# Optimization experiments

Hardware: AMD Instinct MI355X
Metric: run time of the kernel (lower is better)

## Reference

```python
import jax, jax.numpy as jnp
import numpy as np

B, S, D, H = 4, 2048, 256, 8
HD = D // H
SCALE = float(np.sqrt(HD))  # temperature = head_dim ** 0.5


def setup_inputs() -> dict:
    key = jax.random.key(0)
    ks = jax.random.split(key, 12)
    w = lambda k, shape: jax.random.normal(k, shape, dtype=jnp.float32) * 0.05
    x = jax.random.normal(ks[0], (B, S, D), dtype=jnp.float32)
    adj = jax.random.randint(ks[1], (B, S, S), 0, 2, dtype=jnp.int32)
    return {
        "x": x,
        "adj": adj,
        "w_qkv": w(ks[2], (3 * D, D)),
        "b_qkv": jnp.zeros((3 * D,), jnp.float32),
        "ln_g": jnp.ones((D,), jnp.float32),
        "ln_b": jnp.zeros((D,), jnp.float32),
        "w_fc": w(ks[3], (D, D)),
        "b_fc": jnp.zeros((D,), jnp.float32),
        "w_z": w(ks[4], (D, D)),
        "b_z": jnp.full((D,), -2.0, jnp.float32),  # init_bias fills w_z bias with -2
        "u_z": w(ks[5], (D, D)),
        "w_r": w(ks[6], (D, D)),
        "u_r": w(ks[7], (D, D)),
        "w_g": w(ks[8], (D, D)),
        "u_g": w(ks[9], (D, D)),
    }


def reference(x, adj, w_qkv, b_qkv, ln_g, ln_b, w_fc, b_fc,
              w_z, b_z, u_z, w_r, u_r, w_g, u_g):
    residual = x
    # LayerNorm (eps=1e-5, torch default)
    mu = jnp.mean(x, axis=-1, keepdims=True)
    var = jnp.var(x, axis=-1, keepdims=True)
    xn = (x - mu) / jnp.sqrt(var + 1e-5) * ln_g + ln_b
    # fused QKV projection -> (B*H, S, 3*HD), batch-major over (b, h)
    qkv = xn @ w_qkv.T + b_qkv                       # [B,S,3D]
    qkv = qkv.reshape(B, S, H, 3 * HD).transpose(0, 2, 1, 3).reshape(B * H, S, 3 * HD)
    q, k, v = jnp.split(qkv, 3, axis=-1)
    # masked scaled dot-product attention (full NxN scores, as in original)
    attn = jnp.einsum('nqd,nkd->nqk', q, k) / SCALE  # [B*H,S,S]
    adj_r = jnp.repeat(adj, H, axis=0)               # batch-major, matches attn layout
    attn = jnp.where(adj_r == 0, -jnp.inf, attn)
    attn = jax.nn.softmax(attn, axis=-1)
    out = jnp.einsum('nqk,nkd->nqd', attn, v)        # [B*H,S,HD]
    # Faithful replication of torch's view(n_head, batch, ...) applied to
    # batch-major data (an ordering quirk in the original module).
    out = out.reshape(H, B, S, HD).transpose(1, 2, 0, 3).reshape(B, S, D)
    y = jax.nn.relu(out @ w_fc.T + b_fc)
    # GRU gate: x=residual, y=attention branch
    z = jax.nn.sigmoid(y @ w_z.T + b_z + residual @ u_z.T)
    r = jax.nn.sigmoid(y @ w_r.T + residual @ u_r.T)
    h_hat = jnp.tanh(y @ w_g.T + (r * residual) @ u_g.T)
    return (1.0 - z) * residual + z * h_hat
```

## Files before the change

### kernel.cpp

```cpp
#include <hip/hip_runtime.h>
#include <hip/hip_bf16.h>
#include <math.h>

#define B_  4
#define S_  2048
#define D_  256
#define H_  8
#define HD_ 32
#define QSCALE 0.25504175929589786f

typedef short  bf16x8 __attribute__((ext_vector_type(8)));
typedef float  f32x4  __attribute__((ext_vector_type(4)));
typedef float  f32x16 __attribute__((ext_vector_type(16)));
typedef unsigned short ushort_t;
typedef unsigned int   uint_t;

__device__ __forceinline__ ushort_t f2b(float f) {
    union { float f; unsigned u; } v; v.f = f;
    unsigned r = (v.u + 0x7FFFu + ((v.u >> 16) & 1u)) >> 16;
    return (ushort_t)r;
}
__device__ __forceinline__ float b2f(ushort_t s) {
    return __uint_as_float((uint_t)s << 16);
}
__device__ __forceinline__ f32x16 zero16() {
    f32x16 z;
#pragma unroll
    for (int i = 0; i < 16; ++i) z[i] = 0.f;
    return z;
}
__device__ __forceinline__ float wave_allsum(float v) {
#pragma unroll
    for (int o = 32; o > 0; o >>= 1) v += __shfl_xor(v, o, 64);
    return v;
}

#define WQ_SZ 196608
#define WS_SZ 65536
#define NB_WC2 160
#define NB_LN4 2048
__global__ __launch_bounds__(256)
void prep_kernel(const float* __restrict__ w0, const float* __restrict__ w1,
                 const float* __restrict__ w2, const float* __restrict__ w3,
                 const float* __restrict__ w4, const float* __restrict__ w5,
                 const float* __restrict__ w6, const float* __restrict__ w7,
                 ushort_t* __restrict__ wout,
                 const float* __restrict__ x, const float* __restrict__ g,
                 const float* __restrict__ bb, ushort_t* __restrict__ xn_b) {
    __shared__ float T[16][260];
    int blk = blockIdx.x, tid = threadIdx.x;
    if (blk < NB_WC2) {
        const float* src; int ct;
        if (blk < 48) { src = w0; ct = blk; }
        else {
            int j = blk - 48, seg = j >> 4; ct = j & 15;
            src = (seg == 0) ? w1 : (seg == 1) ? w2 : (seg == 2) ? w3 :
                  (seg == 3) ? w4 : (seg == 4) ? w5 : (seg == 5) ? w6 : w7;
        }
#pragma unroll
        for (int p = 0; p < 4; ++p) {
            int u = p * 256 + tid;
            int row = u >> 6, col = (u & 63) * 4;
            float4 v = *(const float4*)(src + (size_t)(ct * 16 + row) * 256 + col);
            T[row][col]     = v.x; T[row][col + 1] = v.y;
            T[row][col + 2] = v.z; T[row][col + 3] = v.w;
        }
        __syncthreads();
        ushort_t* ob = wout + (size_t)blk * 4096;
#pragma unroll
        for (int p = 0; p < 2; ++p) {
            int m = p * 256 + tid;
            int l = m & 15, qd = (m >> 4) & 3, ks = m >> 6;
            const float* tp = &T[l][ks * 32 + qd * 8];
            union { ushort_t u[8]; uint4 q; } pk;
#pragma unroll
            for (int j = 0; j < 8; ++j) pk.u[j] = f2b(tp[j]);
            *(uint4*)(ob + ks * 512 + qd * 128 + l * 8) = pk.q;
        }
    } else {
        int wave = tid >> 6, lane = tid & 63;
        int row = (blk - NB_WC2) * 4 + wave;
        int col = lane * 4;
        float4 t = *(const float4*)(x + (size_t)row * 256 + col);
        float s = wave_allsum(t.x + t.y + t.z + t.w);
        float mu = s * (1.0f / D_);
        float d0 = t.x - mu, d1 = t.y - mu, d2 = t.z - mu, d3 = t.w - mu;
        float v = wave_allsum(d0 * d0 + d1 * d1 + d2 * d2 + d3 * d3);
        float rstd = rsqrtf(v * (1.0f / D_) + 1e-5f);
        float4 gv = *(const float4*)(g + col);
        float4 bv = *(const float4*)(bb + col);
        union { ushort_t u[4]; uint2 q; } o;
        o.u[0] = f2b(d0 * rstd * gv.x + bv.x);
        o.u[1] = f2b(d1 * rstd * gv.y + bv.y);
        o.u[2] = f2b(d2 * rstd * gv.z + bv.z);
        o.u[3] = f2b(d3 * rstd * gv.w + bv.w);
        *(uint2*)(xn_b + (size_t)row * 256 + col) = o.q;
    }
}

__global__ __launch_bounds__(256)
void gemm_qkv(const ushort_t* __restrict__ A, const ushort_t* __restrict__ Wf,
              const float* __restrict__ bias, ushort_t* __restrict__ outb,
              ushort_t* __restrict__ vT, ushort_t* __restrict__ kD,
              const int* __restrict__ adj, uint_t* __restrict__ bits) {
    __shared__ ushort_t Sa[64][264];
    int tid = threadIdx.x;
    int bid = blockIdx.x;
    int grp = bid / 19, r = bid - grp * 19;
    if (r >= 3) {
        int a = grp * 16 + (r - 3);
        int b = a >> 11, q = a & 2047;
        const int4* arow = (const int4*)(adj + (size_t)a * 2048);
        int4 v0 = arow[tid * 2];
        int4 v1 = arow[tid * 2 + 1];
        unsigned byte = (unsigned)(v0.x != 0)        | ((unsigned)(v0.y != 0) << 1)
                      | ((unsigned)(v0.z != 0) << 2) | ((unsigned)(v0.w != 0) << 3)
                      | ((unsigned)(v1.x != 0) << 4) | ((unsigned)(v1.y != 0) << 5)
                      | ((unsigned)(v1.z != 0) << 6) | ((unsigned)(v1.w != 0) << 7);
        unsigned char* lb = (unsigned char*)&Sa[0][0];
        lb[tid] = (unsigned char)byte;
        __syncthreads();
        if (tid < 64) {
            uint_t w = *(const uint_t*)&lb[tid * 4];
            bits[((size_t)b * 64 + tid) * 2048 + q] = w;
        }
        return;
    }
    int gidx = grp * 3 + r;
    int m0 = (gidx / 12) * 64, n0 = (gidx % 12) * 64;

    int wave = tid >> 6, lane = tid & 63, l = lane & 15, quad = lane >> 4;
    int wm = wave >> 1, wn = wave & 1;
    {
#pragma unroll
        for (int j = 0; j < 8; ++j) {
            int u = tid + j * 256;
            int row = u >> 5, c = (u & 31) * 8;
            *(uint4*)&Sa[row][c] = *(const uint4*)(A + (size_t)(m0 + row) * 256 + c);
        }
    }
    __syncthreads();

    bf16x8 af[2][8];
#pragma unroll
    for (int mt = 0; mt < 2; ++mt)
#pragma unroll
        for (int ks = 0; ks < 8; ++ks)
            af[mt][ks] = *(const bf16x8*)&Sa[wm * 32 + mt * 16 + l][ks * 32 + quad * 8];

    f32x4 acc[2][2];
#pragma unroll
    for (int i = 0; i < 2; ++i)
#pragma unroll
        for (int j = 0; j < 2; ++j) acc[i][j] = (f32x4){0.f, 0.f, 0.f, 0.f};

#pragma unroll
    for (int nt = 0; nt < 2; ++nt) {
        int ct = (n0 >> 4) + wn * 2 + nt;
        bf16x8 wfr[8];
#pragma unroll
        for (int ks = 0; ks < 8; ++ks)
            wfr[ks] = *(const bf16x8*)(Wf + (((size_t)ct * 8 + ks) * 64 + lane) * 8);
#pragma unroll
        for (int ks = 0; ks < 8; ++ks) {
            acc[0][nt] = __builtin_amdgcn_mfma_f32_16x16x32_bf16(af[0][ks], wfr[ks], acc[0][nt], 0, 0, 0);
            acc[1][nt] = __builtin_amdgcn_mfma_f32_16x16x32_bf16(af[1][ks], wfr[ks], acc[1][nt], 0, 0, 0);
        }
    }

    __syncthreads();
    ushort_t* So = &Sa[0][0];
#pragma unroll
    for (int nt = 0; nt < 2; ++nt) {
        int col = wn * 32 + nt * 16 + l;
        int gcol = n0 + col;
        float bv = bias[gcol];
        float qs = ((gcol % 96) < 32) ? QSCALE : 1.0f;
#pragma unroll
        for (int mt = 0; mt < 2; ++mt)
#pragma unroll
            for (int r2 = 0; r2 < 4; ++r2) {
                int row = wm * 32 + mt * 16 + quad * 4 + r2;
                So[row * 72 + col] = f2b((acc[mt][nt][r2] + bv) * qs);
            }
    }
    __syncthreads();
    {
        int row = tid >> 2, seg = tid & 3;
        uint4 v0 = *(uint4*)&So[row * 72 + seg * 16];
        uint4 v1 = *(uint4*)&So[row * 72 + seg * 16 + 8];
        ushort_t* op = outb + (size_t)(m0 + row) * 768 + n0 + seg * 16;
        ((uint4*)op)[0] = v0;
        ((uint4*)op)[1] = v1;
    }

    int vs = n0 % 96;

    if (vs != 64) {
        int kloc = (vs == 0) ? 32 : 0;
        int h  = (vs == 0) ? (n0 / 96) : ((n0 - 32) / 96);
        int b  = m0 >> 11;
        int s0 = m0 & (S_ - 1);
        int krow = tid >> 2, kd = (tid & 3) * 8;
        uint4 v = *(uint4*)&So[krow * 72 + kloc + kd];
        *(uint4*)&kD[((size_t)(b * 8 + h) * S_ + s0 + krow) * 32 + kd] = v;
    }

    if (vs != 0) {
        int vloc = (vs == 64) ? 0 : 32;
        int h  = (n0 + vloc) / 96;
        int b  = m0 >> 11;
        int s0 = m0 & (S_ - 1);
        ushort_t* vstage = &Sa[0][0] + 8192;
        {
            int c = tid & 31, seg = tid >> 5;
            ushort_t tmp[8];
#pragma unroll
            for (int i = 0; i < 8; ++i)
                tmp[i] = So[(seg * 8 + i) * 72 + vloc + c];
            uint_t u[4];
#pragma unroll
            for (int i = 0; i < 4; ++i)
                u[i] = (uint_t)tmp[2 * i] | ((uint_t)tmp[2 * i + 1] << 16);
            *(uint4*)&vstage[c * 72 + seg * 8] = make_uint4(u[0], u[1], u[2], u[3]);
        }
        __syncthreads();
        {
            int d = tid >> 3, tseg = tid & 7;
            uint4 v = *(uint4*)&vstage[d * 72 + tseg * 8];
            *(uint4*)&vT[((size_t)(b * 8 + h) * 32 + d) * S_ + s0 + tseg * 8] = v;
        }
    }
}

__global__ __launch_bounds__(512)
void fused_gate(const ushort_t* __restrict__ attn_b, const float* __restrict__ xf,
                const ushort_t* __restrict__ wfc, const ushort_t* __restrict__ wz,
                const ushort_t* __restrict__ uz, const ushort_t* __restrict__ wr,
                const ushort_t* __restrict__ ur, const ushort_t* __restrict__ wg,
                const ushort_t* __restrict__ ug, const float* __restrict__ bfc,
                const float* __restrict__ bz, float* __restrict__ out) {
    __shared__ ushort_t Sa[16][264];
    __shared__ ushort_t Sx[16][264];
    __shared__ ushort_t Sy[16][264];
    __shared__ ushort_t St[16][264];
    int tid = threadIdx.x;
    int wave = tid >> 6, lane = tid & 63, l = lane & 15, quad = lane >> 4;
    int m0 = blockIdx.x * 16;
    int colbase = wave * 32;

    {
        int row = tid >> 5, c0 = (tid & 31) * 8;
        const ushort_t* ap = attn_b + (size_t)(m0 + row) * 256 + c0;
        *(uint4*)&Sa[row][c0] = *((const uint4*)ap);
        const float4* xp = (const float4*)(xf + (size_t)(m0 + row) * 256 + c0);
        float4 f0 = xp[0], f1 = xp[1];
        union { __hip_bfloat162 h[4]; uint4 u; } p0;
        p0.h[0] = __float22bfloat162_rn(make_float2(f0.x, f0.y));
        p0.h[1] = __float22bfloat162_rn(make_float2(f0.z, f0.w));
        p0.h[2] = __float22bfloat162_rn(make_float2(f1.x, f1.y));
        p0.h[3] = __float22bfloat162_rn(make_float2(f1.z, f1.w));
        *(uint4*)&Sx[row][c0] = p0.u;
    }
    __syncthreads();

    {
        bf16x8 af[8];
#pragma unroll
        for (int ks = 0; ks < 8; ++ks)
            af[ks] = *(const bf16x8*)&Sa[l][ks * 32 + quad * 8];
        f32x4 ya[2];
#pragma unroll
        for (int nt = 0; nt < 2; ++nt) ya[nt] = (f32x4){0.f, 0.f, 0.f, 0.f};
#pragma unroll
        for (int nt = 0; nt < 2; ++nt) {
            size_t fb = ((size_t)(wave * 2 + nt) * 8) * 512 + lane * 8;
#pragma unroll
            for (int ks = 0; ks < 8; ++ks) {
                bf16x8 wfr = *(const bf16x8*)(wfc + fb + ks * 512);
                ya[nt] = __builtin_amdgcn_mfma_f32_16x16x32_bf16(af[ks], wfr, ya[nt], 0, 0, 0);
            }
        }
#pragma unroll
        for (int nt = 0; nt < 2; ++nt) {
            int col = colbase + nt * 16 + l;
            float bv = bfc[col];
#pragma unroll
            for (int r = 0; r < 4; ++r)
                Sy[quad * 4 + r][col] = f2b(fmaxf(ya[nt][r] + bv, 0.0f));
        }
    }
    __syncthreads();

    f32x4 az[2], ar[2], ag[2];
#pragma unroll
    for (int nt = 0; nt < 2; ++nt) {
        az[nt] = (f32x4){0.f, 0.f, 0.f, 0.f};
        ar[nt] = (f32x4){0.f, 0.f, 0.f, 0.f};
        ag[nt] = (f32x4){0.f, 0.f, 0.f, 0.f};
    }
#pragma unroll
    for (int nt = 0; nt < 2; ++nt) {
        size_t fb = ((size_t)(wave * 2 + nt) * 8) * 512 + lane * 8;
#pragma unroll
        for (int ks = 0; ks < 8; ++ks) {
            bf16x8 fy = *(const bf16x8*)&Sy[l][ks * 32 + quad * 8];
            bf16x8 fx = *(const bf16x8*)&Sx[l][ks * 32 + quad * 8];
            bf16x8 fz  = *(const bf16x8*)(wz + fb + ks * 512);
            bf16x8 fuz = *(const bf16x8*)(uz + fb + ks * 512);
            bf16x8 fr  = *(const bf16x8*)(wr + fb + ks * 512);
            bf16x8 fur = *(const bf16x8*)(ur + fb + ks * 512);
            bf16x8 fg  = *(const bf16x8*)(wg + fb + ks * 512);
            az[nt] = __builtin_amdgcn_mfma_f32_16x16x32_bf16(fy, fz,  az[nt], 0, 0, 0);
            az[nt] = __builtin_amdgcn_mfma_f32_16x16x32_bf16(fx, fuz, az[nt], 0, 0, 0);
            ar[nt] = __builtin_amdgcn_mfma_f32_16x16x32_bf16(fy, fr,  ar[nt], 0, 0, 0);
            ar[nt] = __builtin_amdgcn_mfma_f32_16x16x32_bf16(fx, fur, ar[nt], 0, 0, 0);
            ag[nt] = __builtin_amdgcn_mfma_f32_16x16x32_bf16(fy, fg,  ag[nt], 0, 0, 0);
        }
    }
#pragma unroll
    for (int nt = 0; nt < 2; ++nt) {
        int col = colbase + nt * 16 + l;
        float bzv = bz[col];
#pragma unroll
        for (int r = 0; r < 4; ++r) {
            int row = quad * 4 + r;
            az[nt][r] = 1.0f / (1.0f + __expf(-(az[nt][r] + bzv)));
            float rr  = 1.0f / (1.0f + __expf(-ar[nt][r]));
            St[row][col] = f2b(rr * b2f(Sx[row][col]));
        }
    }
    __syncthreads();

    f32x4 fcc[2];
#pragma unroll
    for (int nt = 0; nt < 2; ++nt) fcc[nt] = (f32x4){0.f, 0.f, 0.f, 0.f};
#pragma unroll
    for (int nt = 0; nt < 2; ++nt) {
        size_t fb = ((size_t)(wave * 2 + nt) * 8) * 512 + lane * 8;
#pragma unroll
        for (int ks = 0; ks < 8; ++ks) {
            bf16x8 ft = *(const bf16x8*)&St[l][ks * 32 + quad * 8];
            bf16x8 fu = *(const bf16x8*)(ug + fb + ks * 512);
            fcc[nt] = __builtin_amdgcn_mfma_f32_16x16x32_bf16(ft, fu, fcc[nt], 0, 0, 0);
        }
    }
#pragma unroll
    for (int nt = 0; nt < 2; ++nt) {
        int col = colbase + nt * 16 + l;
#pragma unroll
        for (int r = 0; r < 4; ++r) {
            int row = quad * 4 + r;
            float v = ag[nt][r] + fcc[nt][r];
            float e = __expf(2.0f * v);
            float h = 1.0f - 2.0f / (e + 1.0f);
            float zz = az[nt][r];
            size_t idx = (size_t)(m0 + row) * 256 + col;
            out[idx] = (1.0f - zz) * xf[idx] + zz * h;
        }
    }
}

#define ATTN_COMPUTE(CUR, A0, A1)                                                         \
    {                                                                                     \
        _Pragma("unroll")                                                                 \
        for (int kb2 = 0; kb2 < 2; ++kb2) {                                               \
            const int kb = kofs + kb2 * 32;                                               \
            bf16x8 kf1 = *(const bf16x8*)&Ks[CUR][kb + lane5][(hi ^ b3) * 8];             \
            bf16x8 kf2 = *(const bf16x8*)&Ks[CUR][kb + lane5][((2 + hi) ^ b3) * 8];       \
            f32x16 sc = zero16();                                                         \
            sc = __builtin_amdgcn_mfma_f32_32x32x16_bf16(kf1, qf1, sc, 0, 0, 0);          \
            sc = __builtin_amdgcn_mfma_f32_32x32x16_bf16(kf2, qf2, sc, 0, 0, 0);          \
            uint_t wsub = (kb2 ? (A1) : (A0)) >> hsh8;                                    \
            union { uint_t u[8]; bf16x8 v[2]; } pp;                                       \
            _Pragma("unroll")                                                             \
            for (int i = 0; i < 8; ++i) {                                                 \
                const int c = 2 * i + ((i >> 2) * 8);                                     \
                float e0 = __builtin_amdgcn_exp2f(sc[2 * i]);                             \
                float e1 = __builtin_amdgcn_exp2f(sc[2 * i + 1]);                         \
                uint_t mm0 = (uint_t)((int)(wsub << (31 - c)) >> 31);                     \
                uint_t mm1 = (uint_t)((int)(wsub << (30 - c)) >> 31);                     \
                e0 = __uint_as_float(__float_as_uint(e0) & mm0);                          \
                e1 = __uint_as_float(__float_as_uint(e1) & mm1);                          \
                union { __hip_bfloat162 b2; uint_t u; } p;                                \
                p.b2 = __float22bfloat162_rn(make_float2(e0, e1));                        \
                pp.u[i] = p.u;                                                            \
            }                                                                             \
            bf16x8 vb1 = *(const bf16x8*)&Vt[CUR][lane5][kb + hsh8];                      \
            bf16x8 vb2 = *(const bf16x8*)&Vt[CUR][lane5][kb + 16 + hsh8];                 \
            __builtin_amdgcn_s_setprio(1);                                                \
            oacc  = __builtin_amdgcn_mfma_f32_32x32x16_bf16(pp.v[0], vb1,  oacc,  0, 0, 0); \
            aones = __builtin_amdgcn_mfma_f32_32x32x16_bf16(pp.v[0], ones, aones, 0, 0, 0); \
            oacc  = __builtin_amdgcn_mfma_f32_32x32x16_bf16(pp.v[1], vb2,  oacc,  0, 0, 0); \
            aones = __builtin_amdgcn_mfma_f32_32x32x16_bf16(pp.v[1], ones, aones, 0, 0, 0); \
            __builtin_amdgcn_s_setprio(0);                                                \
        }                                                                                 \
    }

__global__ __launch_bounds__(256)
void attn_kernel(const ushort_t* __restrict__ qkvb, const ushort_t* __restrict__ kD,
                 const ushort_t* __restrict__ vT,
                 const uint_t* __restrict__ abits, ushort_t* __restrict__ attn_b) {
    __shared__ ushort_t Ks[2][128][40];
    __shared__ ushort_t Vt[2][32][136];

    int tid = threadIdx.x;
    int wave = tid >> 6, lane = tid & 63;
    int lane5 = lane & 31, hi = lane >> 5;
    int hsh8 = hi * 8;
    int pair = wave >> 1, half = wave & 1;

    int lid = blockIdx.y * 32 + blockIdx.x;
    int L   = (lid & 7) * 128 + (lid >> 3);
    int q0  = (L & 31) * 64;
    int n   = L >> 5;
    int b = n >> 3, h = n & 7;
    int bp = n & 3, hp = n >> 2;

    const ushort_t* base = qkvb + (size_t)b * S_ * 768 + h * 96;
    int qbase = pair * 32;
    int myq = q0 + qbase + lane5;
    const int kofs = half * 64;

    bf16x8 qf1 = *(const bf16x8*)(base + (size_t)myq * 768 + hsh8);
    bf16x8 qf2 = *(const bf16x8*)(base + (size_t)myq * 768 + 16 + hsh8);

    bf16x8 ones;
#pragma unroll
    for (int i = 0; i < 8; ++i) ones[i] = (short)0x3F80;

    f32x16 oacc = zero16(), aones = zero16();

    int skey = tid >> 1, sj = tid & 1;
    int prow = (skey & ~12) | ((skey & 4) << 1) | ((skey & 8) >> 1);
    int pxor = ((prow >> 3) & 1) << 3;
    int vd = tid >> 3, vk = (tid & 7) * 8;
    const ushort_t* vptr = vT + ((size_t)n * 32 + vd) * S_ + vk;
    const ushort_t* kpt  = kD + ((size_t)n * S_ + skey) * 32 + sj * 16;
    const uint_t* tb = abits + ((size_t)b * 64) * 2048 + myq;

    uint_t aw0 = tb[(size_t)(half * 2 + 0) * 2048];
    uint_t aw1 = tb[(size_t)(half * 2 + 1) * 2048];
    {
        uint4 ka = *(const uint4*)(kpt);
        uint4 kb_ = *(const uint4*)(kpt + 8);
        uint4 va = *(const uint4*)(vptr);
        uint4 vb_ = *(const uint4*)(vptr + 64);
        *(uint4*)&Ks[0][prow][(sj * 16 + 0) ^ pxor] = ka;
        *(uint4*)&Ks[0][prow][(sj * 16 + 8) ^ pxor] = kb_;
        *(uint4*)&Vt[0][vd][vk] = va;
        *(uint4*)&Vt[0][vd][vk + 64] = vb_;
    }
    uint4 kv0 = *(const uint4*)(kpt + (size_t)128 * 32);
    uint4 kv1 = *(const uint4*)(kpt + (size_t)128 * 32 + 8);
    uint4 vv0 = *(const uint4*)(vptr + 128);
    uint4 vv1 = *(const uint4*)(vptr + 192);
    __syncthreads();

    int b3 = (lane >> 3) & 1;

#pragma unroll 1
    for (int w = 0; w < 15; ++w) {
        int k0 = w * 128;
        int cur = w & 1;
        *(uint4*)&Ks[cur ^ 1][prow][(sj * 16 + 0) ^ pxor] = kv0;
        *(uint4*)&Ks[cur ^ 1][prow][(sj * 16 + 8) ^ pxor] = kv1;
        *(uint4*)&Vt[cur ^ 1][vd][vk] = vv0;
        *(uint4*)&Vt[cur ^ 1][vd][vk + 64] = vv1;
        int wn = ((k0 + 128) >> 5) + half * 2;
        uint_t awn0 = tb[(size_t)(wn + 0) * 2048];
        uint_t awn1 = tb[(size_t)(wn + 1) * 2048];
        int kpre = (k0 + 256) & (S_ - 1);
        kv0 = *(const uint4*)(kpt + (size_t)kpre * 32);
        kv1 = *(const uint4*)(kpt + (size_t)kpre * 32 + 8);
        vv0 = *(const uint4*)(vptr + kpre);
        vv1 = *(const uint4*)(vptr + kpre + 64);

        ATTN_COMPUTE(cur, aw0, aw1)

        aw0 = awn0; aw1 = awn1;
        __syncthreads();
    }
    ATTN_COMPUTE(1, aw0, aw1)
    __syncthreads();

    float* red = (float*)&Ks[0][0][0];
    if (half) {
        float* dst = red + pair * 2048 + lane * 4;
#pragma unroll
        for (int j = 0; j < 4; ++j) {
            f32x4 t;
            t[0] = oacc[4 * j]; t[1] = oacc[4 * j + 1];
            t[2] = oacc[4 * j + 2]; t[3] = oacc[4 * j + 3];
            *(f32x4*)(dst + j * 256) = t;
        }
#pragma unroll
        for (int j = 0; j < 4; ++j) {
            f32x4 t;
            t[0] = aones[4 * j]; t[1] = aones[4 * j + 1];
            t[2] = aones[4 * j + 2]; t[3] = aones[4 * j + 3];
            *(f32x4*)(dst + (4 + j) * 256) = t;
        }
    }
    __syncthreads();
    if (!half) {
        const float* src = red + pair * 2048 + lane * 4;
#pragma unroll
        for (int j = 0; j < 4; ++j) {
            f32x4 t = *(const f32x4*)(src + j * 256);
            oacc[4 * j] += t[0]; oacc[4 * j + 1] += t[1];
            oacc[4 * j + 2] += t[2]; oacc[4 * j + 3] += t[3];
        }
#pragma unroll
        for (int j = 0; j < 4; ++j) {
            f32x4 t = *(const f32x4*)(src + (4 + j) * 256);
            aones[4 * j] += t[0]; aones[4 * j + 1] += t[1];
            aones[4 * j + 2] += t[2]; aones[4 * j + 3] += t[3];
        }
    }
    __syncthreads();

    ushort_t* Ost = &Ks[0][0][0];
    if (!half) {
#pragma unroll
        for (int r = 0; r < 16; ++r) {
            int qr = (r & 3) + 8 * (r >> 2) + 4 * hi;
            Ost[(qbase + qr) * 40 + lane5] = f2b(oacc[r] / aones[r]);
        }
    }
    __syncthreads();
    {
        int row = tid >> 2, part = tid & 3;
        uint4 v = *(uint4*)&Ost[row * 40 + part * 8];
        *(uint4*)&attn_b[((size_t)(bp * S_ + q0 + row)) * 256 + hp * 32 + part * 8] = v;
    }
}

extern "C" void kernel_launch(void* const* d_in, const int* in_sizes, int n_in,
                              void* d_out, int out_size, void* d_ws, size_t ws_size,
                              hipStream_t stream) {
    const float* x     = (const float*)d_in[0];
    const int*   adj   = (const int*)d_in[1];
    const float* w_qkv = (const float*)d_in[2];
    const float* b_qkv = (const float*)d_in[3];
    const float* ln_g  = (const float*)d_in[4];
    const float* ln_b  = (const float*)d_in[5];
    const float* w_fc  = (const float*)d_in[6];
    const float* b_fc  = (const float*)d_in[7];
    const float* w_z   = (const float*)d_in[8];
    const float* b_z   = (const float*)d_in[9];
    const float* u_z   = (const float*)d_in[10];
    const float* w_r   = (const float*)d_in[11];
    const float* u_r   = (const float*)d_in[12];
    const float* w_g   = (const float*)d_in[13];
    const float* u_g   = (const float*)d_in[14];
    float* out = (float*)d_out;

    const size_t TOK  = (size_t)B_ * S_;
    const size_t TOKD = TOK * D_;
    ushort_t* xn_b   = (ushort_t*)d_ws;
    ushort_t* qkv_b  = xn_b + TOKD;
    ushort_t* attn_b = qkv_b + TOK * 768;
    ushort_t* wb     = attn_b + TOKD;
    uint_t*   bits   = (uint_t*)(wb + WQ_SZ + 7 * WS_SZ);
    ushort_t* vTb    = (ushort_t*)(bits + (size_t)B_ * S_ * S_ / 32);
    ushort_t* kDb    = vTb + (size_t)32 * 32 * S_;

    ushort_t* wq_b  = wb;
    ushort_t* wfc_b = wb + WQ_SZ;
    ushort_t* wz_b  = wfc_b + WS_SZ;
    ushort_t* uz_b  = wz_b + WS_SZ;
    ushort_t* wr_b  = uz_b + WS_SZ;
    ushort_t* ur_b  = wr_b + WS_SZ;
    ushort_t* wg_b  = ur_b + WS_SZ;
    ushort_t* ug_b  = wg_b + WS_SZ;

    prep_kernel<<<NB_WC2 + NB_LN4, 256, 0, stream>>>(
        w_qkv, w_fc, w_z, u_z, w_r, u_r, w_g, u_g, wb,
        x, ln_g, ln_b, xn_b);

    gemm_qkv<<<9728, 256, 0, stream>>>(xn_b, wq_b, b_qkv, qkv_b, vTb, kDb, adj, bits);

    attn_kernel<<<dim3(S_ / 64, B_ * H_), 256, 0, stream>>>(qkv_b, kDb, vTb, bits, attn_b);

    fused_gate<<<512, 512, 0, stream>>>(
        attn_b, x, wfc_b, wz_b, uz_b, wr_b, ur_b, wg_b, ug_b, b_fc, b_z, out);
}
```

Baseline: 207.9 us.

## Move gate weight conversion into attention grid and double gate row tile

Gate-weight bf16 conversion blocks are appended to the attention kernel grid, so that conversion overlaps attention work instead of lengthening the prep kernel. The fused gate kernel now processes 32 rows per block with two M-tiles, reusing each global weight fragment load across both tiles and halving the grid. This raises register and LDS use per block and reduces the number of gate blocks available to fill the GPU.

After: 208.7 us. No clear change (+0.4%).

```diff
diff --git a/kernel.cpp b/kernel.cpp
--- a/kernel.cpp
+++ b/kernel.cpp
@@ -37,31 +37,21 @@
 
 #define WQ_SZ 196608
 #define WS_SZ 65536
-#define NB_WC2 160
+#define NB_WQ  48
 #define NB_LN4 2048
 __global__ __launch_bounds__(256)
-void prep_kernel(const float* __restrict__ w0, const float* __restrict__ w1,
-                 const float* __restrict__ w2, const float* __restrict__ w3,
-                 const float* __restrict__ w4, const float* __restrict__ w5,
-                 const float* __restrict__ w6, const float* __restrict__ w7,
-                 ushort_t* __restrict__ wout,
+void prep_kernel(const float* __restrict__ w0, ushort_t* __restrict__ wout,
                  const float* __restrict__ x, const float* __restrict__ g,
                  const float* __restrict__ bb, ushort_t* __restrict__ xn_b) {
     __shared__ float T[16][260];
     int blk = blockIdx.x, tid = threadIdx.x;
-    if (blk < NB_WC2) {
-        const float* src; int ct;
-        if (blk < 48) { src = w0; ct = blk; }
-        else {
-            int j = blk - 48, seg = j >> 4; ct = j & 15;
-            src = (seg == 0) ? w1 : (seg == 1) ? w2 : (seg == 2) ? w3 :
-                  (seg == 3) ? w4 : (seg == 4) ? w5 : (seg == 5) ? w6 : w7;
-        }
+    if (blk < NB_WQ) {
+        int ct = blk;
 #pragma unroll
         for (int p = 0; p < 4; ++p) {
             int u = p * 256 + tid;
             int row = u >> 6, col = (u & 63) * 4;
-            float4 v = *(const float4*)(src + (size_t)(ct * 16 + row) * 256 + col);
+            float4 v = *(const float4*)(w0 + (size_t)(ct * 16 + row) * 256 + col);
             T[row][col]     = v.x; T[row][col + 1] = v.y;
             T[row][col + 2] = v.z; T[row][col + 3] = v.w;
         }
@@ -79,7 +69,7 @@
         }
     } else {
         int wave = tid >> 6, lane = tid & 63;
-        int row = (blk - NB_WC2) * 4 + wave;
+        int row = (blk - NB_WQ) * 4 + wave;
         int col = lane * 4;
         float4 t = *(const float4*)(x + (size_t)row * 256 + col);
         float s = wave_allsum(t.x + t.y + t.z + t.w);
@@ -240,82 +230,103 @@
                 const ushort_t* __restrict__ ur, const ushort_t* __restrict__ wg,
                 const ushort_t* __restrict__ ug, const float* __restrict__ bfc,
                 const float* __restrict__ bz, float* __restrict__ out) {
-    __shared__ ushort_t Sa[16][264];
-    __shared__ ushort_t Sx[16][264];
-    __shared__ ushort_t Sy[16][264];
-    __shared__ ushort_t St[16][264];
+    __shared__ ushort_t Sa[32][264];
+    __shared__ ushort_t Sx[32][264];
+    __shared__ ushort_t Sy[32][264];
+    auto St = Sa;
     int tid = threadIdx.x;
     int wave = tid >> 6, lane = tid & 63, l = lane & 15, quad = lane >> 4;
-    int m0 = blockIdx.x * 16;
+    int m0 = blockIdx.x * 32;
     int colbase = wave * 32;
 
     {
-        int row = tid >> 5, c0 = (tid & 31) * 8;
+        int row = tid >> 4, c0 = (tid & 15) * 16;
         const ushort_t* ap = attn_b + (size_t)(m0 + row) * 256 + c0;
-        *(uint4*)&Sa[row][c0] = *((const uint4*)ap);
+        uint4 a0 = ((const uint4*)ap)[0];
+        uint4 a1 = ((const uint4*)ap)[1];
+        *(uint4*)&Sa[row][c0] = a0;
+        *(uint4*)&Sa[row][c0 + 8] = a1;
         const float4* xp = (const float4*)(xf + (size_t)(m0 + row) * 256 + c0);
-        float4 f0 = xp[0], f1 = xp[1];
-        union { __hip_bfloat162 h[4]; uint4 u; } p0;
+        float4 f0 = xp[0], f1 = xp[1], f2_ = xp[2], f3 = xp[3];
+        union { __hip_bfloat162 h[4]; uint4 u; } p0, p1;
         p0.h[0] = __float22bfloat162_rn(make_float2(f0.x, f0.y));
         p0.h[1] = __float22bfloat162_rn(make_float2(f0.z, f0.w));
         p0.h[2] = __float22bfloat162_rn(make_float2(f1.x, f1.y));
         p0.h[3] = __float22bfloat162_rn(make_float2(f1.z, f1.w));
-        *(uint4*)&Sx[row][c0] = p0.u;
+        p1.h[0] = __float22bfloat162_rn(make_float2(f2_.x, f2_.y));
+        p1.h[1] = __float22bfloat162_rn(make_float2(f2_.z, f2_.w));
+        p1.h[2] = __float22bfloat162_rn(make_float2(f3.x, f3.y));
+        p1.h[3] = __float22bfloat162_rn(make_float2(f3.z, f3.w));
+        *(uint4*)&Sx[row][c0]     = p0.u;
+        *(uint4*)&Sx[row][c0 + 8] = p1.u;
     }
     __syncthreads();
 
     {
-        bf16x8 af[8];
-#pragma unroll
-        for (int ks = 0; ks < 8; ++ks)
-            af[ks] = *(const bf16x8*)&Sa[l][ks * 32 + quad * 8];
-        f32x4 ya[2];
-#pragma unroll
-        for (int nt = 0; nt < 2; ++nt) ya[nt] = (f32x4){0.f, 0.f, 0.f, 0.f};
+        f32x4 ya[2][2];
+#pragma unroll
+        for (int mt = 0; mt < 2; ++mt)
+#pragma unroll
+            for (int nt = 0; nt < 2; ++nt) ya[mt][nt] = (f32x4){0.f, 0.f, 0.f, 0.f};
 #pragma unroll
         for (int nt = 0; nt < 2; ++nt) {
             size_t fb = ((size_t)(wave * 2 + nt) * 8) * 512 + lane * 8;
 #pragma unroll
             for (int ks = 0; ks < 8; ++ks) {
                 bf16x8 wfr = *(const bf16x8*)(wfc + fb + ks * 512);
-                ya[nt] = __builtin_amdgcn_mfma_f32_16x16x32_bf16(af[ks], wfr, ya[nt], 0, 0, 0);
+                bf16x8 a0 = *(const bf16x8*)&Sa[l][ks * 32 + quad * 8];
+                bf16x8 a1 = *(const bf16x8*)&Sa[16 + l][ks * 32 + quad * 8];
+                ya[0][nt] = __builtin_amdgcn_mfma_f32_16x16x32_bf16(a0, wfr, ya[0][nt], 0, 0, 0);
+                ya[1][nt] = __builtin_amdgcn_mfma_f32_16x16x32_bf16(a1, wfr, ya[1][nt], 0, 0, 0);
             }
         }
+        __syncthreads();
 #pragma unroll
         for (int nt = 0; nt < 2; ++nt) {
             int col = colbase + nt * 16 + l;
             float bv = bfc[col];
 #pragma unroll
-            for (int r = 0; r < 4; ++r)
-                Sy[quad * 4 + r][col] = f2b(fmaxf(ya[nt][r] + bv, 0.0f));
-        }
-    }
-    __syncthreads();
-
-    f32x4 az[2], ar[2], ag[2];
-#pragma unroll
-    for (int nt = 0; nt < 2; ++nt) {
-        az[nt] = (f32x4){0.f, 0.f, 0.f, 0.f};
-        ar[nt] = (f32x4){0.f, 0.f, 0.f, 0.f};
-        ag[nt] = (f32x4){0.f, 0.f, 0.f, 0.f};
-    }
+            for (int mt = 0; mt < 2; ++mt)
+#pragma unroll
+                for (int r = 0; r < 4; ++r)
+                    Sy[mt * 16 + quad * 4 + r][col] = f2b(fmaxf(ya[mt][nt][r] + bv, 0.0f));
+        }
+    }
+    __syncthreads();
+
+    f32x4 az[2][2], ar[2][2], ag[2][2];
+#pragma unroll
+    for (int mt = 0; mt < 2; ++mt)
+#pragma unroll
+        for (int nt = 0; nt < 2; ++nt) {
+            az[mt][nt] = (f32x4){0.f, 0.f, 0.f, 0.f};
+            ar[mt][nt] = (f32x4){0.f, 0.f, 0.f, 0.f};
+            ag[mt][nt] = (f32x4){0.f, 0.f, 0.f, 0.f};
+        }
 #pragma unroll
     for (int nt = 0; nt < 2; ++nt) {
         size_t fb = ((size_t)(wave * 2 + nt) * 8) * 512 + lane * 8;
 #pragma unroll
         for (int ks = 0; ks < 8; ++ks) {
-            bf16x8 fy = *(const bf16x8*)&Sy[l][ks * 32 + quad * 8];
-            bf16x8 fx = *(const bf16x8*)&Sx[l][ks * 32 + quad * 8];
             bf16x8 fz  = *(const bf16x8*)(wz + fb + ks * 512);
             bf16x8 fuz = *(const bf16x8*)(uz + fb + ks * 512);
             bf16x8 fr  = *(const bf16x8*)(wr + fb + ks * 512);
             bf16x8 fur = *(const bf16x8*)(ur + fb + ks * 512);
             bf16x8 fg  = *(const bf16x8*)(wg + fb + ks * 512);
-            az[nt] = __builtin_amdgcn_mfma_f32_16x16x32_bf16(fy, fz,  az[nt], 0, 0, 0);
-            az[nt] = __builtin_amdgcn_mfma_f32_16x16x32_bf16(fx, fuz, az[nt], 0, 0, 0);
-            ar[nt] = __builtin_amdgcn_mfma_f32_16x16x32_bf16(fy, fr,  ar[nt], 0, 0, 0);
-            ar[nt] = __builtin_amdgcn_mfma_f32_16x16x32_bf16(fx, fur, ar[nt], 0, 0, 0);
-            ag[nt] = __builtin_amdgcn_mfma_f32_16x16x32_bf16(fy, fg,  ag[nt], 0, 0, 0);
+            bf16x8 fy0 = *(const bf16x8*)&Sy[l][ks * 32 + quad * 8];
+            bf16x8 fy1 = *(const bf16x8*)&Sy[16 + l][ks * 32 + quad * 8];
+            bf16x8 fx0 = *(const bf16x8*)&Sx[l][ks * 32 + quad * 8];
+            bf16x8 fx1 = *(const bf16x8*)&Sx[16 + l][ks * 32 + quad * 8];
+            az[0][nt] = __builtin_amdgcn_mfma_f32_16x16x32_bf16(fy0, fz,  az[0][nt], 0, 0, 0);
+            az[0][nt] = __builtin_amdgcn_mfma_f32_16x16x32_bf16(fx0, fuz, az[0][nt], 0, 0, 0);
+            az[1][nt] = __builtin_amdgcn_mfma_f32_16x16x32_bf16(fy1, fz,  az[1][nt], 0, 0, 0);
+            az[1][nt] = __builtin_amdgcn_mfma_f32_16x16x32_bf16(fx1, fuz, az[1][nt], 0, 0, 0);
+            ar[0][nt] = __builtin_amdgcn_mfma_f32_16x16x32_bf16(fy0, fr,  ar[0][nt], 0, 0, 0);
+            ar[0][nt] = __builtin_amdgcn_mfma_f32_16x16x32_bf16(fx0, fur, ar[0][nt], 0, 0, 0);
+            ar[1][nt] = __builtin_amdgcn_mfma_f32_16x16x32_bf16(fy1, fr,  ar[1][nt], 0, 0, 0);
+            ar[1][nt] = __builtin_amdgcn_mfma_f32_16x16x32_bf16(fx1, fur, ar[1][nt], 0, 0, 0);
+            ag[0][nt] = __builtin_amdgcn_mfma_f32_16x16x32_bf16(fy0, fg,  ag[0][nt], 0, 0, 0);
+            ag[1][nt] = __builtin_amdgcn_mfma_f32_16x16x32_bf16(fy1, fg,  ag[1][nt], 0, 0, 0);
         }
     }
 #pragma unroll
@@ -323,41 +334,49 @@
         int col = colbase + nt * 16 + l;
         float bzv = bz[col];
 #pragma unroll
-        for (int r = 0; r < 4; ++r) {
-            int row = quad * 4 + r;
-            az[nt][r] = 1.0f / (1.0f + __expf(-(az[nt][r] + bzv)));
-            float rr  = 1.0f / (1.0f + __expf(-ar[nt][r]));
-            St[row][col] = f2b(rr * b2f(Sx[row][col]));
-        }
-    }
-    __syncthreads();
-
-    f32x4 fcc[2];
-#pragma unroll
-    for (int nt = 0; nt < 2; ++nt) fcc[nt] = (f32x4){0.f, 0.f, 0.f, 0.f};
+        for (int mt = 0; mt < 2; ++mt)
+#pragma unroll
+            for (int r = 0; r < 4; ++r) {
+                int row = mt * 16 + quad * 4 + r;
+                az[mt][nt][r] = 1.0f / (1.0f + __expf(-(az[mt][nt][r] + bzv)));
+                float rr  = 1.0f / (1.0f + __expf(-ar[mt][nt][r]));
+                St[row][col] = f2b(rr * b2f(Sx[row][col]));
+            }
+    }
+    __syncthreads();
+
+    f32x4 fcc[2][2];
+#pragma unroll
+    for (int mt = 0; mt < 2; ++mt)
+#pragma unroll
+        for (int nt = 0; nt < 2; ++nt) fcc[mt][nt] = (f32x4){0.f, 0.f, 0.f, 0.f};
 #pragma unroll
     for (int nt = 0; nt < 2; ++nt) {
         size_t fb = ((size_t)(wave * 2 + nt) * 8) * 512 + lane * 8;
 #pragma unroll
         for (int ks = 0; ks < 8; ++ks) {
-            bf16x8 ft = *(const bf16x8*)&St[l][ks * 32 + quad * 8];
-            bf16x8 fu = *(const bf16x8*)(ug + fb + ks * 512);
-            fcc[nt] = __builtin_amdgcn_mfma_f32_16x16x32_bf16(ft, fu, fcc[nt], 0, 0, 0);
+            bf16x8 fu  = *(const bf16x8*)(ug + fb + ks * 512);
+            bf16x8 ft0 = *(const bf16x8*)&St[l][ks * 32 + quad * 8];
+            bf16x8 ft1 = *(const bf16x8*)&St[16 + l][ks * 32 + quad * 8];
+            fcc[0][nt] = __builtin_amdgcn_mfma_f32_16x16x32_bf16(ft0, fu, fcc[0][nt], 0, 0, 0);
+            fcc[1][nt] = __builtin_amdgcn_mfma_f32_16x16x32_bf16(ft1, fu, fcc[1][nt], 0, 0, 0);
         }
     }
 #pragma unroll
     for (int nt = 0; nt < 2; ++nt) {
         int col = colbase + nt * 16 + l;
 #pragma unroll
-        for (int r = 0; r < 4; ++r) {
-            int row = quad * 4 + r;
-            float v = ag[nt][r] + fcc[nt][r];
-            float e = __expf(2.0f * v);
-            float h = 1.0f - 2.0f / (e + 1.0f);
-            float zz = az[nt][r];
-            size_t idx = (size_t)(m0 + row) * 256 + col;
-            out[idx] = (1.0f - zz) * xf[idx] + zz * h;
-        }
+        for (int mt = 0; mt < 2; ++mt)
+#pragma unroll
+            for (int r = 0; r < 4; ++r) {
+                int row = mt * 16 + quad * 4 + r;
+                float v = ag[mt][nt][r] + fcc[mt][nt][r];
+                float e = __expf(2.0f * v);
+                float h = 1.0f - 2.0f / (e + 1.0f);
+                float zz = az[mt][nt][r];
+                size_t idx = (size_t)(m0 + row) * 256 + col;
+                out[idx] = (1.0f - zz) * xf[idx] + zz * h;
+            }
     }
 }
 
@@ -400,17 +419,51 @@
 __global__ __launch_bounds__(256)
 void attn_kernel(const ushort_t* __restrict__ qkvb, const ushort_t* __restrict__ kD,
                  const ushort_t* __restrict__ vT,
-                 const uint_t* __restrict__ abits, ushort_t* __restrict__ attn_b) {
+                 const uint_t* __restrict__ abits, ushort_t* __restrict__ attn_b,
+                 const float* __restrict__ gw0, const float* __restrict__ gw1,
+                 const float* __restrict__ gw2, const float* __restrict__ gw3,
+                 const float* __restrict__ gw4, const float* __restrict__ gw5,
+                 const float* __restrict__ gw6, ushort_t* __restrict__ wout) {
     __shared__ ushort_t Ks[2][128][40];
     __shared__ ushort_t Vt[2][32][136];
 
     int tid = threadIdx.x;
+    int lid = blockIdx.x;
+
+    if (lid >= 1024) {
+        int wblk = lid - 1024;
+        int seg = wblk >> 4, ct = wblk & 15;
+        const float* src = (seg == 0) ? gw0 : (seg == 1) ? gw1 : (seg == 2) ? gw2 :
+                           (seg == 3) ? gw3 : (seg == 4) ? gw4 : (seg == 5) ? gw5 : gw6;
+        float* T = (float*)&Ks[0][0][0];
+#pragma unroll
+        for (int p = 0; p < 4; ++p) {
+            int u = p * 256 + tid;
+            int row = u >> 6, col = (u & 63) * 4;
+            float4 v = *(const float4*)(src + (size_t)(ct * 16 + row) * 256 + col);
+            T[row * 260 + col]     = v.x; T[row * 260 + col + 1] = v.y;
+            T[row * 260 + col + 2] = v.z; T[row * 260 + col + 3] = v.w;
+        }
+        __syncthreads();
+        ushort_t* ob = wout + (size_t)(48 + wblk) * 4096;
+#pragma unroll
+        for (int p = 0; p < 2; ++p) {
+            int m = p * 256 + tid;
+            int l2 = m & 15, qd = (m >> 4) & 3, ks2 = m >> 6;
+            const float* tp = &T[l2 * 260 + ks2 * 32 + qd * 8];
+            union { ushort_t u[8]; uint4 q; } pk;
+#pragma unroll
+            for (int j = 0; j < 8; ++j) pk.u[j] = f2b(tp[j]);
+            *(uint4*)(ob + ks2 * 512 + qd * 128 + l2 * 8) = pk.q;
+        }
+        return;
+    }
+
     int wave = tid >> 6, lane = tid & 63;
     int lane5 = lane & 31, hi = lane >> 5;
     int hsh8 = hi * 8;
     int pair = wave >> 1, half = wave & 1;
 
-    int lid = blockIdx.y * 32 + blockIdx.x;
     int L   = (lid & 7) * 128 + (lid >> 3);
     int q0  = (L & 31) * 64;
     int n   = L >> 5;
@@ -575,14 +628,14 @@
     ushort_t* wg_b  = ur_b + WS_SZ;
     ushort_t* ug_b  = wg_b + WS_SZ;
 
-    prep_kernel<<<NB_WC2 + NB_LN4, 256, 0, stream>>>(
-        w_qkv, w_fc, w_z, u_z, w_r, u_r, w_g, u_g, wb,
-        x, ln_g, ln_b, xn_b);
+    prep_kernel<<<NB_WQ + NB_LN4, 256, 0, stream>>>(
+        w_qkv, wb, x, ln_g, ln_b, xn_b);
 
     gemm_qkv<<<9728, 256, 0, stream>>>(xn_b, wq_b, b_qkv, qkv_b, vTb, kDb, adj, bits);
 
-    attn_kernel<<<dim3(S_ / 64, B_ * H_), 256, 0, stream>>>(qkv_b, kDb, vTb, bits, attn_b);
-
-    fused_gate<<<512, 512, 0, stream>>>(
+    attn_kernel<<<1136, 256, 0, stream>>>(qkv_b, kDb, vTb, bits, attn_b,
+                                          w_fc, w_z, u_z, w_r, u_r, w_g, u_g, wb);
+
+    fused_gate<<<256, 512, 0, stream>>>(
         attn_b, x, wfc_b, wz_b, uz_b, wr_b, ur_b, wg_b, ug_b, b_fc, b_z, out);
 }
```
